# Performance work log

Measured on AMD Instinct MI355X. Metric: run time of the kernel, lower is better.

## Reference

```python
import jax, jax.numpy as jnp
import numpy as np

TEMPERATURE = 0.5
EPS = 1e-8  # torch F.cosine_similarity norm clamp


def setup_inputs() -> dict:
    key = jax.random.key(0)
    k1, k2 = jax.random.split(key)
    N, D = 4096, 256
    z1 = jax.random.normal(k1, (N, D), dtype=jnp.float32)
    z2 = jax.random.normal(k2, (N, D), dtype=jnp.float32)
    return {"z1": z1, "z2": z2}


def _l2norm(x):
    # matches torch cosine_similarity eps clamping on the norm
    n = jnp.sqrt(jnp.sum(x * x, axis=-1, keepdims=True))
    return x / jnp.maximum(n, EPS)


def reference(z1, z2):
    N = z1.shape[0]
    f = jnp.concatenate([z1, z2], axis=0)          # [2N, D]
    fn = _l2norm(f)                                 # row-normalized
    sim = fn @ fn.T                                 # [2N, 2N] cosine similarities
    diag = jnp.eye(2 * N, dtype=bool)
    # denominator: sum over off-diagonal entries (self-similarity excluded)
    denom = jnp.sum(jnp.where(diag, 0.0, jnp.exp(sim / TEMPERATURE)), axis=1)  # [2N]
    # positives: cosine(z1_i, z2_i), duplicated for both views
    z1n, z2n = _l2norm(z1), _l2norm(z2)
    pos = jnp.sum(z1n * z2n, axis=1)               # [N]
    pos = jnp.concatenate([pos, pos], axis=0)      # [2N]
    loss = -jnp.mean(jnp.log(jnp.exp(pos / TEMPERATURE) / denom))
    return loss
```

## Files before the change

### kernel.cpp

```cpp
#include <hip/hip_runtime.h>
#include <hip/hip_fp8.h>

#define D 256
#define SCALE 1.69864354f
#define EPS 1e-8f

typedef __attribute__((ext_vector_type(4))) float f32x4;
typedef long fp8x8;

__global__ __launch_bounds__(256) void normpos_kernel(
    const float* __restrict__ z1, const float* __restrict__ z2,
    unsigned char* __restrict__ fnq, float* __restrict__ pos,
    int* __restrict__ sync, int N) {
  if (blockIdx.x == 0 && threadIdx.x == 0) *sync = 0;
  int wid  = threadIdx.x >> 6;
  int lane = threadIdx.x & 63;
  int row  = blockIdx.x * 4 + wid;
  f32x4 a = *(const f32x4*)(z1 + (size_t)row * D + lane * 4);
  f32x4 b = *(const f32x4*)(z2 + (size_t)row * D + lane * 4);
  float s1  = a.x * a.x + a.y * a.y + a.z * a.z + a.w * a.w;
  float s2  = b.x * b.x + b.y * b.y + b.z * b.z + b.w * b.w;
  float dot = a.x * b.x + a.y * b.y + a.z * b.z + a.w * b.w;
  #pragma unroll
  for (int m = 1; m < 64; m <<= 1) {
    s1  += __shfl_xor(s1, m, 64);
    s2  += __shfl_xor(s2, m, 64);
    dot += __shfl_xor(dot, m, 64);
  }
  float inv1 = 1.0f / fmaxf(sqrtf(s1), EPS);
  float inv2 = 1.0f / fmaxf(sqrtf(s2), EPS);
  float q1 = inv1 * SCALE, q2 = inv2 * SCALE;
  unsigned int w1 = 0, w2 = 0;
  #pragma unroll
  for (int j = 0; j < 4; ++j) {
    w1 |= (unsigned int)__hip_cvt_float_to_fp8(a[j] * q1, __HIP_SATFINITE,
                                               __HIP_E4M3) << (8 * j);
    w2 |= (unsigned int)__hip_cvt_float_to_fp8(b[j] * q2, __HIP_SATFINITE,
                                               __HIP_E4M3) << (8 * j);
  }
  *(unsigned int*)(fnq + (size_t)row * D + lane * 4)       = w1;
  *(unsigned int*)(fnq + (size_t)(N + row) * D + lane * 4) = w2;
  if (lane == 0) pos[row] = dot * inv1 * inv2;
}


__device__ __forceinline__ void stage_tile(const unsigned char* __restrict__ row0,
                                           int kk, unsigned char* lds, int tid) {
  #pragma unroll
  for (int it = 0; it < 4; ++it) {
    int s = it * 256 + tid;
    int r = s >> 3;
    int p = s & 7;
    const unsigned char* src =
        row0 + (size_t)r * D + kk * 128 + ((p ^ (r & 7)) << 4);
    __builtin_amdgcn_global_load_lds(
        (const __attribute__((address_space(1))) void*)src,
        (__attribute__((address_space(3))) void*)(lds + s * 16), 16, 0, 0);
  }
}

__global__ __launch_bounds__(256, 4) void denom_kernel(
    const unsigned char* __restrict__ fnq, float* __restrict__ partial,
    int twoN) {
  __shared__ unsigned char As[128 * 128];
  __shared__ unsigned char Bs[128 * 128];
  __shared__ float redR[128][2];
  __shared__ float redC[128][2];

  int tid  = threadIdx.x;
  int wid  = tid >> 6;
  int lane = tid & 63;
  int c = lane & 15;
  int g = lane >> 4;
  int wr = wid >> 1, wc = wid & 1;

  int chunkpx = (int)gridDim.x >> 3;
  int bid = (blockIdx.x & 7) * chunkpx + (blockIdx.x >> 3);

  int i = (int)((sqrtf(8.f * (float)bid + 1.f) - 1.f) * 0.5f);
  while ((i + 1) * (i + 2) / 2 <= bid) ++i;
  while (i * (i + 1) / 2 > bid) --i;
  int rb = bid - i * (i + 1) / 2;
  int cb = i;
  const unsigned char* Arow0 = fnq + (size_t)rb * 128 * D;
  const unsigned char* Brow0 = fnq + (size_t)cb * 128 * D;

  bool dblk  = (rb == cb);
  bool dwave = dblk && (wr == wc);

  f32x4 acc[4][4] = {};

  stage_tile(Arow0, 0, As, tid);
  stage_tile(Brow0, 0, Bs, tid);

  #pragma unroll
  for (int kk = 0; kk < 2; ++kk) {
    __syncthreads();
    #pragma unroll
    for (int ks = 0; ks < 4; ++ks) {
      fp8x8 a[4], b[4];
      int q  = (ks << 1) | (g >> 1);
      int h  = (g & 1) << 3;
      #pragma unroll
      for (int mi = 0; mi < 4; ++mi) {
        int ar = wr * 64 + mi * 16 + c;
        a[mi] = *(const fp8x8*)(As + ar * 128 + ((q ^ (ar & 7)) << 4) + h);
      }
      #pragma unroll
      for (int ni = 0; ni < 4; ++ni) {
        int bc = wc * 64 + ni * 16 + c;
        b[ni] = *(const fp8x8*)(Bs + bc * 128 + ((q ^ (bc & 7)) << 4) + h);
      }
      #pragma unroll
      for (int mi = 0; mi < 4; ++mi)
        #pragma unroll
        for (int ni = 0; ni < 4; ++ni)
          acc[mi][ni] = __builtin_amdgcn_mfma_f32_16x16x32_fp8_fp8(
              a[mi], b[ni], acc[mi][ni], 0, 0, 0);
    }
    if (kk == 0) {
      __syncthreads();
      stage_tile(Arow0, 1, As, tid);
      stage_tile(Brow0, 1, Bs, tid);
    }
  }

  float rsum[16];
  float csum[4];
  #pragma unroll
  for (int ii = 0; ii < 16; ++ii) rsum[ii] = 0.f;
  #pragma unroll
  for (int ii = 0; ii < 4; ++ii) csum[ii] = 0.f;

  if (dwave) {
    #pragma unroll
    for (int mi = 0; mi < 4; ++mi)
      #pragma unroll
      for (int ni = 0; ni < 4; ++ni) {
        int colloc = ni * 16 + c;
        #pragma unroll
        for (int r = 0; r < 4; ++r) {
          int rowloc = mi * 16 + g * 4 + r;
          float e = __builtin_amdgcn_exp2f(acc[mi][ni][r]);
          if (rowloc == colloc) e = 0.f;
          rsum[mi * 4 + r] += e;
        }
      }
  } else if (dblk) {
    #pragma unroll
    for (int mi = 0; mi < 4; ++mi)
      #pragma unroll
      for (int ni = 0; ni < 4; ++ni)
        #pragma unroll
        for (int r = 0; r < 4; ++r)
          rsum[mi * 4 + r] += __builtin_amdgcn_exp2f(acc[mi][ni][r]);
  } else {
    #pragma unroll
    for (int mi = 0; mi < 4; ++mi)
      #pragma unroll
      for (int ni = 0; ni < 4; ++ni)
        #pragma unroll
        for (int r = 0; r < 4; ++r) {
          float e = __builtin_amdgcn_exp2f(acc[mi][ni][r]);
          rsum[mi * 4 + r] += e;
          csum[ni]         += e;
        }
  }

  #pragma unroll
  for (int ii = 0; ii < 16; ++ii) {
    float v = rsum[ii];
    v += __shfl_xor(v, 1, 64);
    v += __shfl_xor(v, 2, 64);
    v += __shfl_xor(v, 4, 64);
    v += __shfl_xor(v, 8, 64);
    rsum[ii] = v;
  }
  if (c == 0) {
    #pragma unroll
    for (int mi = 0; mi < 4; ++mi)
      #pragma unroll
      for (int r = 0; r < 4; ++r)
        redR[wr * 64 + mi * 16 + g * 4 + r][wc] = rsum[mi * 4 + r];
  }
  if (!dblk) {
    #pragma unroll
    for (int ii = 0; ii < 4; ++ii) {
      float v = csum[ii];
      v += __shfl_xor(v, 16, 64);
      v += __shfl_xor(v, 32, 64);
      csum[ii] = v;
    }
    if (g == 0) {
      #pragma unroll
      for (int ni = 0; ni < 4; ++ni)
        redC[wc * 64 + ni * 16 + c][wr] = csum[ni];
    }
  }
  __syncthreads();
  if (tid < 128) {
    partial[(size_t)cb * twoN + rb * 128 + tid] =
        redR[tid][0] + redR[tid][1];
    if (rb != cb)
      partial[(size_t)rb * twoN + cb * 128 + tid] =
          redC[tid][0] + redC[tid][1];
  }
}

__global__ __launch_bounds__(256) void reduce_kernel(
    const float* __restrict__ partial, const float* __restrict__ pos,
    float* __restrict__ bsum, float* __restrict__ out, int* __restrict__ sync,
    int twoN, int N, int nsplit) {
  int row = blockIdx.x * 256 + threadIdx.x;
  int wid = threadIdx.x >> 6, lane = threadIdx.x & 63;
  float denom = 0.f;
  for (int s = 0; s < nsplit; ++s) denom += partial[(size_t)s * twoN + row];
  float ld = logf(denom);
  float p  = (row < N) ? pos[row] : 0.f;
  #pragma unroll
  for (int m = 1; m < 64; m <<= 1) {
    ld += __shfl_xor(ld, m, 64);
    p  += __shfl_xor(p, m, 64);
  }
  __shared__ float sld[4], spo[4];
  __shared__ int lastf;
  if (lane == 0) { sld[wid] = ld; spo[wid] = p; }
  __syncthreads();
  if (threadIdx.x == 0) {
    bsum[blockIdx.x]             = sld[0] + sld[1] + sld[2] + sld[3];
    bsum[gridDim.x + blockIdx.x] = spo[0] + spo[1] + spo[2] + spo[3];
    __threadfence();
    lastf = (atomicAdd(sync, 1) == (int)gridDim.x - 1);
  }
  __syncthreads();
  if (lastf && threadIdx.x < 64) {
    __threadfence();
    int t = threadIdx.x;
    int nb = gridDim.x;
    float l2 = (t < nb) ? bsum[t] : 0.f;
    float p2 = (t < nb) ? bsum[nb + t] : 0.f;
    #pragma unroll
    for (int m = 1; m < 64; m <<= 1) {
      l2 += __shfl_xor(l2, m, 64);
      p2 += __shfl_xor(p2, m, 64);
    }
    if (t == 0) out[0] = l2 / (float)twoN - 2.f * (p2 / (float)N);
  }
}

extern "C" void kernel_launch(void* const* d_in, const int* in_sizes, int n_in,
                              void* d_out, int out_size, void* d_ws,
                              size_t ws_size, hipStream_t stream) {
  const float* z1 = (const float*)d_in[0];
  const float* z2 = (const float*)d_in[1];
  int N = in_sizes[0] / D;
  int twoN = 2 * N;
  int nrb = twoN / 128;

  unsigned char* fnq = (unsigned char*)d_ws;
  float* partial = (float*)((char*)d_ws + (size_t)twoN * D);
  float* pos     = (float*)((char*)partial + (size_t)nrb * twoN * 4);
  float* bsum    = (float*)((char*)pos + (size_t)N * 4);
  int*   sync    = (int*)((char*)bsum + 256 * 4);

  normpos_kernel<<<N / 4, 256, 0, stream>>>(z1, z2, fnq, pos, sync, N);
  int ntri = nrb * (nrb + 1) / 2;
  denom_kernel<<<ntri, 256, 0, stream>>>(fnq, partial, twoN);
  int nblk = twoN / 256;
  reduce_kernel<<<nblk, 256, 0, stream>>>(partial, pos, bsum, (float*)d_out,
                                          sync, twoN, N, nrb);
}
```

Baseline: 53.63 us.

## Fuse final reduction into denom kernel via atomic row accumulation

Replaces the per-tile partial-sum matrix and the separate reduce kernel with float atomicAdds into a single row-denominator array, zeroed in the normalization kernel. The last-finishing denom block, detected through an atomic counter, computes the log-sum and positive-sum and writes the loss. This removes one kernel launch and the partial-buffer traffic. In exchange it adds atomic contention, a serial tail in one block, and non-deterministic float summation order. The XCD-aware block remapping is also dropped.

```diff
diff --git a/kernel.cpp b/kernel.cpp
--- a/kernel.cpp
+++ b/kernel.cpp
@@ -11,8 +11,9 @@
 __global__ __launch_bounds__(256) void normpos_kernel(
     const float* __restrict__ z1, const float* __restrict__ z2,
     unsigned char* __restrict__ fnq, float* __restrict__ pos,
-    int* __restrict__ sync, int N) {
+    float* __restrict__ denomacc, int* __restrict__ sync, int N) {
   if (blockIdx.x == 0 && threadIdx.x == 0) *sync = 0;
+  if (blockIdx.x < 32) denomacc[blockIdx.x * 256 + threadIdx.x] = 0.f;
   int wid  = threadIdx.x >> 6;
   int lane = threadIdx.x & 63;
   int row  = blockIdx.x * 4 + wid;
@@ -60,8 +61,9 @@
 }
 
 __global__ __launch_bounds__(256, 4) void denom_kernel(
-    const unsigned char* __restrict__ fnq, float* __restrict__ partial,
-    int twoN) {
+    const unsigned char* __restrict__ fnq, float* __restrict__ denomacc,
+    const float* __restrict__ pos, float* __restrict__ out,
+    int* __restrict__ sync, int twoN, int N, int ntri) {
   __shared__ unsigned char As[128 * 128];
   __shared__ unsigned char Bs[128 * 128];
   __shared__ float redR[128][2];
@@ -74,9 +76,7 @@
   int g = lane >> 4;
   int wr = wid >> 1, wc = wid & 1;
 
-  int chunkpx = (int)gridDim.x >> 3;
-  int bid = (blockIdx.x & 7) * chunkpx + (blockIdx.x >> 3);
-
+  int bid = blockIdx.x;
   int i = (int)((sqrtf(8.f * (float)bid + 1.f) - 1.f) * 0.5f);
   while ((i + 1) * (i + 2) / 2 <= bid) ++i;
   while (i * (i + 1) / 2 > bid) --i;
@@ -199,52 +199,34 @@
   }
   __syncthreads();
   if (tid < 128) {
-    partial[(size_t)cb * twoN + rb * 128 + tid] =
-        redR[tid][0] + redR[tid][1];
+    atomicAdd(denomacc + rb * 128 + tid, redR[tid][0] + redR[tid][1]);
     if (rb != cb)
-      partial[(size_t)rb * twoN + cb * 128 + tid] =
-          redC[tid][0] + redC[tid][1];
-  }
-}
-
-__global__ __launch_bounds__(256) void reduce_kernel(
-    const float* __restrict__ partial, const float* __restrict__ pos,
-    float* __restrict__ bsum, float* __restrict__ out, int* __restrict__ sync,
-    int twoN, int N, int nsplit) {
-  int row = blockIdx.x * 256 + threadIdx.x;
-  int wid = threadIdx.x >> 6, lane = threadIdx.x & 63;
-  float denom = 0.f;
-  for (int s = 0; s < nsplit; ++s) denom += partial[(size_t)s * twoN + row];
-  float ld = logf(denom);
-  float p  = (row < N) ? pos[row] : 0.f;
-  #pragma unroll
-  for (int m = 1; m < 64; m <<= 1) {
-    ld += __shfl_xor(ld, m, 64);
-    p  += __shfl_xor(p, m, 64);
-  }
-  __shared__ float sld[4], spo[4];
+      atomicAdd(denomacc + cb * 128 + tid, redC[tid][0] + redC[tid][1]);
+  }
+  __syncthreads();
+
   __shared__ int lastf;
-  if (lane == 0) { sld[wid] = ld; spo[wid] = p; }
+  if (tid == 0) {
+    __threadfence();
+    lastf = (atomicAdd(sync, 1) == ntri - 1);
+  }
   __syncthreads();
-  if (threadIdx.x == 0) {
-    bsum[blockIdx.x]             = sld[0] + sld[1] + sld[2] + sld[3];
-    bsum[gridDim.x + blockIdx.x] = spo[0] + spo[1] + spo[2] + spo[3];
+  if (lastf) {
     __threadfence();
-    lastf = (atomicAdd(sync, 1) == (int)gridDim.x - 1);
-  }
-  __syncthreads();
-  if (lastf && threadIdx.x < 64) {
-    __threadfence();
-    int t = threadIdx.x;
-    int nb = gridDim.x;
-    float l2 = (t < nb) ? bsum[t] : 0.f;
-    float p2 = (t < nb) ? bsum[nb + t] : 0.f;
+    float ls = 0.f, ps = 0.f;
+    for (int r = tid; r < twoN; r += 256) ls += logf(denomacc[r]);
+    for (int r = tid; r < N; r += 256) ps += pos[r];
     #pragma unroll
     for (int m = 1; m < 64; m <<= 1) {
-      l2 += __shfl_xor(l2, m, 64);
-      p2 += __shfl_xor(p2, m, 64);
-    }
-    if (t == 0) out[0] = l2 / (float)twoN - 2.f * (p2 / (float)N);
+      ls += __shfl_xor(ls, m, 64);
+      ps += __shfl_xor(ps, m, 64);
+    }
+    __shared__ float sl[4], sp[4];
+    if (lane == 0) { sl[wid] = ls; sp[wid] = ps; }
+    __syncthreads();
+    if (tid == 0)
+      out[0] = (sl[0] + sl[1] + sl[2] + sl[3]) / (float)twoN -
+               2.f * (sp[0] + sp[1] + sp[2] + sp[3]) / (float)N;
   }
 }
 
@@ -255,18 +237,15 @@
   const float* z2 = (const float*)d_in[1];
   int N = in_sizes[0] / D;
   int twoN = 2 * N;
+
+  unsigned char* fnq = (unsigned char*)d_ws;
+  float* denomacc = (float*)((char*)d_ws + (size_t)twoN * D);
+  float* pos      = (float*)((char*)denomacc + (size_t)twoN * 4);
+  int*   sync     = (int*)((char*)pos + (size_t)N * 4);
+
+  normpos_kernel<<<N / 4, 256, 0, stream>>>(z1, z2, fnq, pos, denomacc, sync, N);
   int nrb = twoN / 128;
-
-  unsigned char* fnq = (unsigned char*)d_ws;
-  float* partial = (float*)((char*)d_ws + (size_t)twoN * D);
-  float* pos     = (float*)((char*)partial + (size_t)nrb * twoN * 4);
-  float* bsum    = (float*)((char*)pos + (size_t)N * 4);
-  int*   sync    = (int*)((char*)bsum + 256 * 4);
-
-  normpos_kernel<<<N / 4, 256, 0, stream>>>(z1, z2, fnq, pos, sync, N);
   int ntri = nrb * (nrb + 1) / 2;
-  denom_kernel<<<ntri, 256, 0, stream>>>(fnq, partial, twoN);
-  int nblk = twoN / 256;
-  reduce_kernel<<<nblk, 256, 0, stream>>>(partial, pos, bsum, (float*)d_out,
-                                          sync, twoN, N, nrb);
-}
+  denom_kernel<<<ntri, 256, 0, stream>>>(fnq, denomacc, pos, (float*)d_out,
+                                         sync, twoN, N, ntri);
+}
```

New measurement: 79.28 us. +47.8%, slower.

## Process two triangle tiles per block with double-buffered 64-wide K staging

Applied to the files above, without the earlier changes.

The denominator kernel now has each block handle two consecutive upper-triangle tiles, halving the grid. The K dimension is staged in 64-byte slices into two ping-pong LDS buffers, so the next slice or the next tile's data loads while MFMAs and the exp/reduction epilogue of the current tile run. The XCD-aware block remapping is dropped, which may reduce L2 locality. Each block now serialises two tiles, so per-block latency grows in exchange for overlapping load and compute and fewer block launches.

```diff
diff --git a/kernel.cpp b/kernel.cpp
--- a/kernel.cpp
+++ b/kernel.cpp
@@ -44,15 +44,15 @@
 }
 
 
-__device__ __forceinline__ void stage_tile(const unsigned char* __restrict__ row0,
-                                           int kk, unsigned char* lds, int tid) {
-  #pragma unroll
-  for (int it = 0; it < 4; ++it) {
+__device__ __forceinline__ void stage64(const unsigned char* __restrict__ row0,
+                                        int kk, unsigned char* lds, int tid) {
+  #pragma unroll
+  for (int it = 0; it < 2; ++it) {
     int s = it * 256 + tid;
-    int r = s >> 3;
-    int p = s & 7;
+    int r = s >> 2;
+    int p = s & 3;
     const unsigned char* src =
-        row0 + (size_t)r * D + kk * 128 + ((p ^ (r & 7)) << 4);
+        row0 + (size_t)r * D + kk * 64 + ((p ^ (r & 3)) << 4);
     __builtin_amdgcn_global_load_lds(
         (const __attribute__((address_space(1))) void*)src,
         (__attribute__((address_space(3))) void*)(lds + s * 16), 16, 0, 0);
@@ -62,8 +62,8 @@
 __global__ __launch_bounds__(256, 4) void denom_kernel(
     const unsigned char* __restrict__ fnq, float* __restrict__ partial,
     int twoN) {
-  __shared__ unsigned char As[128 * 128];
-  __shared__ unsigned char Bs[128 * 128];
+  __shared__ unsigned char As[2][128 * 64];
+  __shared__ unsigned char Bs[2][128 * 64];
   __shared__ float redR[128][2];
   __shared__ float redC[128][2];
 
@@ -74,42 +74,49 @@
   int g = lane >> 4;
   int wr = wid >> 1, wc = wid & 1;
 
-  int chunkpx = (int)gridDim.x >> 3;
-  int bid = (blockIdx.x & 7) * chunkpx + (blockIdx.x >> 3);
-
-  int i = (int)((sqrtf(8.f * (float)bid + 1.f) - 1.f) * 0.5f);
-  while ((i + 1) * (i + 2) / 2 <= bid) ++i;
-  while (i * (i + 1) / 2 > bid) --i;
-  int rb = bid - i * (i + 1) / 2;
-  int cb = i;
-  const unsigned char* Arow0 = fnq + (size_t)rb * 128 * D;
-  const unsigned char* Brow0 = fnq + (size_t)cb * 128 * D;
-
-  bool dblk  = (rb == cb);
-  bool dwave = dblk && (wr == wc);
+  int rbs[2], cbs[2];
+  #pragma unroll
+  for (int j = 0; j < 2; ++j) {
+    int bid = 2 * blockIdx.x + j;
+    int i = (int)((sqrtf(8.f * (float)bid + 1.f) - 1.f) * 0.5f);
+    while ((i + 1) * (i + 2) / 2 <= bid) ++i;
+    while (i * (i + 1) / 2 > bid) --i;
+    rbs[j] = bid - i * (i + 1) / 2;
+    cbs[j] = i;
+  }
+  const unsigned char* Ar[2] = {fnq + (size_t)rbs[0] * 128 * D,
+                                fnq + (size_t)rbs[1] * 128 * D};
+  const unsigned char* Br[2] = {fnq + (size_t)cbs[0] * 128 * D,
+                                fnq + (size_t)cbs[1] * 128 * D};
+
+  stage64(Ar[0], 0, As[0], tid);
+  stage64(Br[0], 0, Bs[0], tid);
+  __syncthreads();
 
   f32x4 acc[4][4] = {};
-
-  stage_tile(Arow0, 0, As, tid);
-  stage_tile(Brow0, 0, Bs, tid);
-
-  #pragma unroll
-  for (int kk = 0; kk < 2; ++kk) {
-    __syncthreads();
+  #pragma unroll
+  for (int u = 0; u < 8; ++u) {
+    const int j  = u >> 2;
+    const int kk = u & 3;
+    const int cur = u & 1;
+    if (u < 7) {
+      stage64(Ar[(u + 1) >> 2], (u + 1) & 3, As[cur ^ 1], tid);
+      stage64(Br[(u + 1) >> 2], (u + 1) & 3, Bs[cur ^ 1], tid);
+    }
     #pragma unroll
-    for (int ks = 0; ks < 4; ++ks) {
+    for (int ks = 0; ks < 2; ++ks) {
       fp8x8 a[4], b[4];
-      int q  = (ks << 1) | (g >> 1);
-      int h  = (g & 1) << 3;
+      int q = (ks << 1) | (g >> 1);
+      int h = (g & 1) << 3;
       #pragma unroll
       for (int mi = 0; mi < 4; ++mi) {
         int ar = wr * 64 + mi * 16 + c;
-        a[mi] = *(const fp8x8*)(As + ar * 128 + ((q ^ (ar & 7)) << 4) + h);
+        a[mi] = *(const fp8x8*)(As[cur] + ar * 64 + ((q ^ (ar & 3)) << 4) + h);
       }
       #pragma unroll
       for (int ni = 0; ni < 4; ++ni) {
         int bc = wc * 64 + ni * 16 + c;
-        b[ni] = *(const fp8x8*)(Bs + bc * 128 + ((q ^ (bc & 7)) << 4) + h);
+        b[ni] = *(const fp8x8*)(Bs[cur] + bc * 64 + ((q ^ (bc & 3)) << 4) + h);
       }
       #pragma unroll
       for (int mi = 0; mi < 4; ++mi)
@@ -118,92 +125,93 @@
           acc[mi][ni] = __builtin_amdgcn_mfma_f32_16x16x32_fp8_fp8(
               a[mi], b[ni], acc[mi][ni], 0, 0, 0);
     }
-    if (kk == 0) {
-      __syncthreads();
-      stage_tile(Arow0, 1, As, tid);
-      stage_tile(Brow0, 1, Bs, tid);
-    }
-  }
-
-  float rsum[16];
-  float csum[4];
-  #pragma unroll
-  for (int ii = 0; ii < 16; ++ii) rsum[ii] = 0.f;
-  #pragma unroll
-  for (int ii = 0; ii < 4; ++ii) csum[ii] = 0.f;
-
-  if (dwave) {
-    #pragma unroll
-    for (int mi = 0; mi < 4; ++mi)
-      #pragma unroll
-      for (int ni = 0; ni < 4; ++ni) {
-        int colloc = ni * 16 + c;
-        #pragma unroll
-        for (int r = 0; r < 4; ++r) {
-          int rowloc = mi * 16 + g * 4 + r;
-          float e = __builtin_amdgcn_exp2f(acc[mi][ni][r]);
-          if (rowloc == colloc) e = 0.f;
-          rsum[mi * 4 + r] += e;
+    if (kk == 3) {
+      bool dblk  = (rbs[j] == cbs[j]);
+      bool dwave = dblk && (wr == wc);
+      float rsum[16];
+      float csum[4];
+      #pragma unroll
+      for (int ii = 0; ii < 16; ++ii) rsum[ii] = 0.f;
+      #pragma unroll
+      for (int ii = 0; ii < 4; ++ii) csum[ii] = 0.f;
+      if (dwave) {
+        #pragma unroll
+        for (int mi = 0; mi < 4; ++mi)
+          #pragma unroll
+          for (int ni = 0; ni < 4; ++ni) {
+            int colloc = ni * 16 + c;
+            #pragma unroll
+            for (int r = 0; r < 4; ++r) {
+              int rowloc = mi * 16 + g * 4 + r;
+              float e = __builtin_amdgcn_exp2f(acc[mi][ni][r]);
+              if (rowloc == colloc) e = 0.f;
+              rsum[mi * 4 + r] += e;
+            }
+          }
+      } else if (dblk) {
+        #pragma unroll
+        for (int mi = 0; mi < 4; ++mi)
+          #pragma unroll
+          for (int ni = 0; ni < 4; ++ni)
+            #pragma unroll
+            for (int r = 0; r < 4; ++r)
+              rsum[mi * 4 + r] += __builtin_amdgcn_exp2f(acc[mi][ni][r]);
+      } else {
+        #pragma unroll
+        for (int mi = 0; mi < 4; ++mi)
+          #pragma unroll
+          for (int ni = 0; ni < 4; ++ni)
+            #pragma unroll
+            for (int r = 0; r < 4; ++r) {
+              float e = __builtin_amdgcn_exp2f(acc[mi][ni][r]);
+              rsum[mi * 4 + r] += e;
+              csum[ni]         += e;
+            }
+      }
+      #pragma unroll
+      for (int ii = 0; ii < 16; ++ii) {
+        float v = rsum[ii];
+        v += __shfl_xor(v, 1, 64);
+        v += __shfl_xor(v, 2, 64);
+        v += __shfl_xor(v, 4, 64);
+        v += __shfl_xor(v, 8, 64);
+        rsum[ii] = v;
+      }
+      if (c == 0) {
+        #pragma unroll
+        for (int mi = 0; mi < 4; ++mi)
+          #pragma unroll
+          for (int r = 0; r < 4; ++r)
+            redR[wr * 64 + mi * 16 + g * 4 + r][wc] = rsum[mi * 4 + r];
+      }
+      if (!dblk) {
+        #pragma unroll
+        for (int ii = 0; ii < 4; ++ii) {
+          float v = csum[ii];
+          v += __shfl_xor(v, 16, 64);
+          v += __shfl_xor(v, 32, 64);
+          csum[ii] = v;
         }
-      }
-  } else if (dblk) {
-    #pragma unroll
-    for (int mi = 0; mi < 4; ++mi)
-      #pragma unroll
-      for (int ni = 0; ni < 4; ++ni)
-        #pragma unroll
-        for (int r = 0; r < 4; ++r)
-          rsum[mi * 4 + r] += __builtin_amdgcn_exp2f(acc[mi][ni][r]);
-  } else {
-    #pragma unroll
-    for (int mi = 0; mi < 4; ++mi)
-      #pragma unroll
-      for (int ni = 0; ni < 4; ++ni)
-        #pragma unroll
-        for (int r = 0; r < 4; ++r) {
-          float e = __builtin_amdgcn_exp2f(acc[mi][ni][r]);
-          rsum[mi * 4 + r] += e;
-          csum[ni]         += e;
+        if (g == 0) {
+          #pragma unroll
+          for (int ni = 0; ni < 4; ++ni)
+            redC[wc * 64 + ni * 16 + c][wr] = csum[ni];
         }
-  }
-
-  #pragma unroll
-  for (int ii = 0; ii < 16; ++ii) {
-    float v = rsum[ii];
-    v += __shfl_xor(v, 1, 64);
-    v += __shfl_xor(v, 2, 64);
-    v += __shfl_xor(v, 4, 64);
-    v += __shfl_xor(v, 8, 64);
-    rsum[ii] = v;
-  }
-  if (c == 0) {
-    #pragma unroll
-    for (int mi = 0; mi < 4; ++mi)
-      #pragma unroll
-      for (int r = 0; r < 4; ++r)
-        redR[wr * 64 + mi * 16 + g * 4 + r][wc] = rsum[mi * 4 + r];
-  }
-  if (!dblk) {
-    #pragma unroll
-    for (int ii = 0; ii < 4; ++ii) {
-      float v = csum[ii];
-      v += __shfl_xor(v, 16, 64);
-      v += __shfl_xor(v, 32, 64);
-      csum[ii] = v;
-    }
-    if (g == 0) {
-      #pragma unroll
-      for (int ni = 0; ni < 4; ++ni)
-        redC[wc * 64 + ni * 16 + c][wr] = csum[ni];
-    }
-  }
-  __syncthreads();
-  if (tid < 128) {
-    partial[(size_t)cb * twoN + rb * 128 + tid] =
-        redR[tid][0] + redR[tid][1];
-    if (rb != cb)
-      partial[(size_t)rb * twoN + cb * 128 + tid] =
-          redC[tid][0] + redC[tid][1];
+      }
+      #pragma unroll
+      for (int mi = 0; mi < 4; ++mi)
+        #pragma unroll
+        for (int ni = 0; ni < 4; ++ni)
+          acc[mi][ni] = f32x4{0.f, 0.f, 0.f, 0.f};
+    }
+    __syncthreads();
+    if (kk == 3 && tid < 128) {
+      partial[(size_t)cbs[j] * twoN + rbs[j] * 128 + tid] =
+          redR[tid][0] + redR[tid][1];
+      if (rbs[j] != cbs[j])
+        partial[(size_t)rbs[j] * twoN + cbs[j] * 128 + tid] =
+            redC[tid][0] + redC[tid][1];
+    }
   }
 }
 
@@ -265,7 +273,7 @@
 
   normpos_kernel<<<N / 4, 256, 0, stream>>>(z1, z2, fnq, pos, sync, N);
   int ntri = nrb * (nrb + 1) / 2;
-  denom_kernel<<<ntri, 256, 0, stream>>>(fnq, partial, twoN);
+  denom_kernel<<<ntri / 2, 256, 0, stream>>>(fnq, partial, twoN);
   int nblk = twoN / 256;
   reduce_kernel<<<nblk, 256, 0, stream>>>(partial, pos, bsum, (float*)d_out,
                                           sync, twoN, N, nrb);
```

New measurement: 69.61 us. 1.3x slower.
